# Kernel tuning notes

Measured on AMD Instinct MI355X. Metric: run time of the kernel, lower is better.

## Reference

```python
import jax, jax.numpy as jnp
import numpy as np

D, H = 1024, 8
HD = D // H           # head_dim = 128
M1 = 64               # att_mid_dim[1]
ALPHA = 1.3           # CELU alpha
EPS = 1e-5            # GroupNorm eps


def celu(x):
    return jnp.where(x > 0, x, ALPHA * jnp.expm1(x / ALPHA))


def group_norm(x, gamma, beta):
    # torch.nn.GroupNorm(H, D) on 2D input [N, D]: normalize within each group of HD channels
    N, C = x.shape
    xg = x.reshape(N, H, C // H)
    mu = xg.mean(-1, keepdims=True)
    var = xg.var(-1, keepdims=True)
    xn = ((xg - mu) * jax.lax.rsqrt(var + EPS)).reshape(N, C)
    return xn * gamma + beta


def branch(x, W, b, gamma, beta):
    # Linear -> CELU -> GroupNorm
    return group_norm(celu(x @ W + b), gamma, beta)


def setup_inputs() -> dict:
    key = jax.random.key(0)
    ks = jax.random.split(key, 24)
    B, M = 64, 1024
    s = 0.02
    inp = {
        "query": jax.random.normal(ks[0], (B, D), jnp.float32),
        "key": jax.random.normal(ks[1], (B, M, D), jnp.float32),
        "mask": jnp.ones((B, M), jnp.float32),
        "value1": jax.random.normal(ks[2], (B, D), jnp.float32),
        "value2": jax.random.normal(ks[3], (B, M, D), jnp.float32),
    }
    # four Linear+GroupNorm branches
    for i, name in enumerate(["q", "k", "v1", "v2"]):
        inp[f"W{name}"] = jax.random.normal(ks[4 + i], (D, D), jnp.float32) * s
        inp[f"b{name}"] = jnp.zeros((D,), jnp.float32)
        inp[f"g{name}"] = jnp.ones((D,), jnp.float32)
        inp[f"gb{name}"] = jnp.zeros((D,), jnp.float32)
    # SCAttention params: basic Linear(HD->M1), last Linear(M1->1), last2 Linear(M1->HD)
    inp["Wb"] = jax.random.normal(ks[10], (HD, M1), jnp.float32) * s
    inp["bb"] = jnp.zeros((M1,), jnp.float32)
    inp["Wl"] = jax.random.normal(ks[11], (M1, 1), jnp.float32) * s
    inp["bl"] = jnp.zeros((1,), jnp.float32)
    inp["Wl2"] = jax.random.normal(ks[12], (M1, HD), jnp.float32) * s
    inp["bl2"] = jnp.zeros((HD,), jnp.float32)
    return inp


def reference(query, key, mask, value1, value2,
              Wq, bq, gq, gbq, Wk, bk, gk, gbk,
              Wv1, bv1, gv1, gbv1, Wv2, bv2, gv2, gbv2,
              Wb, bb, Wl, bl, Wl2, bl2):
    B = query.shape[0]
    q = branch(query, Wq, bq, gq, gbq).reshape(B, H, HD)           # [B,H,HD]
    v1 = branch(value1, Wv1, bv1, gv1, gbv1).reshape(B, H, HD)     # [B,H,HD]
    k = branch(key.reshape(-1, D), Wk, bk, gk, gbk)
    k = k.reshape(B, -1, H, HD).transpose(0, 2, 1, 3)              # [B,H,M,HD]
    v2 = branch(value2.reshape(-1, D), Wv2, bv2, gv2, gbv2)
    v2 = v2.reshape(B, -1, H, HD).transpose(0, 2, 1, 3)            # [B,H,M,HD]

    attn_map = q[:, :, None, :] * k                                # Hadamard, [B,H,M,HD]

    # SCAttention (eval mode, dropout off)
    am = jax.nn.relu(attn_map @ Wb + bb)                           # [B,H,M,M1]
    mask_e = mask[:, None, :, None]                                # [B,1,M,1]
    am_pool = (am * mask_e).sum(-2) / mask_e.sum(-2)               # [B,H,M1]
    alpha_spatial = (am @ Wl + bl)[..., 0]                         # [B,H,M]
    alpha_channel = jax.nn.sigmoid(am_pool @ Wl2 + bl2)            # [B,H,HD]
    alpha_spatial = jnp.where(mask[:, None, :] == 0, -1e9, alpha_spatial)
    alpha_spatial = jax.nn.softmax(alpha_spatial, axis=-1)
    pooled_v2 = jnp.einsum('bhm,bhmd->bhd', alpha_spatial, v2)     # [B,H,HD]
    attn = v1 * pooled_v2 * alpha_channel                          # [B,H,HD]
    return attn.reshape(B, H * HD)
```

## Files before the change

### kernel.cpp

```cpp
#include <hip/hip_runtime.h>

typedef unsigned short u16;
typedef __attribute__((ext_vector_type(8))) short s16x8;
typedef __attribute__((ext_vector_type(8))) unsigned short u16x8;
typedef __attribute__((ext_vector_type(4))) float f32x4;

#define AS1 __attribute__((address_space(1)))
#define AS3 __attribute__((address_space(3)))

__device__ __forceinline__ float bf2f(u16 u) {
  union { unsigned u; float f; } x; x.u = ((unsigned)u) << 16; return x.f;
}
__device__ __forceinline__ u16 f2bf(float f) {
  union { float f; unsigned u; } x; x.f = f;
  unsigned r = x.u + 0x7fffu + ((x.u >> 16) & 1u);
  return (u16)(r >> 16);
}
__device__ __forceinline__ float celu_f(float x) {
  return x > 0.f ? x : 1.3f * expm1f(x * (1.0f / 1.3f));
}

__global__ __launch_bounds__(256) void convert_bf16(
    const float* __restrict__ X, u16* __restrict__ Y, long n)
{
  long i = ((long)blockIdx.x * 256 + threadIdx.x) * 8;
  const long stride = (long)gridDim.x * 256 * 8;
  for (; i < n; i += stride) {
    f32x4 a = *(const f32x4*)(X + i);
    f32x4 b = *(const f32x4*)(X + i + 4);
    u16x8 t;
#pragma unroll
    for (int e = 0; e < 4; ++e) { t[e] = f2bf(a[e]); t[4 + e] = f2bf(b[e]); }
    *(u16x8*)(Y + i) = t;
  }
}

__global__ __launch_bounds__(256) void transpose2_bf16(
    const float* __restrict__ W0, u16* __restrict__ WT0,
    const float* __restrict__ W1, u16* __restrict__ WT1)
{
  __shared__ float tile[32][33];
  const int bx = blockIdx.x;
  const int sel = blockIdx.y >> 5;
  const int by = blockIdx.y & 31;
  const float* W = sel ? W1 : W0;
  u16* WT = sel ? WT1 : WT0;
  const int tx = threadIdx.x, ty = threadIdx.y;
#pragma unroll
  for (int i = ty; i < 32; i += 8)
    tile[i][tx] = W[(by * 32 + i) * 1024 + bx * 32 + tx];
  __syncthreads();
#pragma unroll
  for (int i = ty; i < 32; i += 8)
    WT[(bx * 32 + i) * 1024 + by * 32 + tx] = f2bf(tile[tx][i]);
}

__global__ __launch_bounds__(256) void transpose_bf16(
    const float* __restrict__ W, u16* __restrict__ WT, int R, int C)
{
  __shared__ float tile[32][33];
  const int bx = blockIdx.x, by = blockIdx.y;
  const int tx = threadIdx.x, ty = threadIdx.y;
#pragma unroll
  for (int i = ty; i < 32; i += 8)
    tile[i][tx] = W[(by * 32 + i) * C + bx * 32 + tx];
  __syncthreads();
#pragma unroll
  for (int i = ty; i < 32; i += 8)
    WT[(bx * 32 + i) * R + by * 32 + tx] = f2bf(tile[tx][i]);
}

__global__ __launch_bounds__(128) void branch_small2(
    const float* __restrict__ X0, const float* __restrict__ W0,
    const float* __restrict__ b0, const float* __restrict__ g0,
    const float* __restrict__ be0, float* __restrict__ o0,
    const float* __restrict__ X1, const float* __restrict__ W1,
    const float* __restrict__ b1, const float* __restrict__ g1,
    const float* __restrict__ be1, float* __restrict__ o1)
{
  const int bid = blockIdx.x;
  const int sel = bid >> 9;
  const float* X = sel ? X1 : X0;  const float* W = sel ? W1 : W0;
  const float* bias = sel ? b1 : b0; const float* gamma = sel ? g1 : g0;
  const float* beta = sel ? be1 : be0; float* out = sel ? o1 : o0;
  const int b = (bid & 511) >> 3, grp = bid & 7;
  const int t = threadIdx.x;
  __shared__ float xs[1024];
  __shared__ float r1[2], r2[2];
  for (int i = t; i < 1024; i += 128) xs[i] = X[b * 1024 + i];
  __syncthreads();
  const int col = grp * 128 + t;
  const float* wp = W + col;
  float a0 = 0.f, a1 = 0.f, a2 = 0.f, a3 = 0.f;
  for (int k = 0; k < 1024; k += 4) {
    a0 += xs[k]     * wp[(k)     * 1024];
    a1 += xs[k + 1] * wp[(k + 1) * 1024];
    a2 += xs[k + 2] * wp[(k + 2) * 1024];
    a3 += xs[k + 3] * wp[(k + 3) * 1024];
  }
  float x = (a0 + a1) + (a2 + a3) + bias[col];
  float c = celu_f(x);
  float s1 = c, s2 = c * c;
#pragma unroll
  for (int m = 1; m < 64; m <<= 1) { s1 += __shfl_xor(s1, m); s2 += __shfl_xor(s2, m); }
  const int w = t >> 6;
  if ((t & 63) == 0) { r1[w] = s1; r2[w] = s2; }
  __syncthreads();
  float t1 = r1[0] + r1[1], t2 = r2[0] + r2[1];
  float mean = t1 * 0.0078125f;
  float var  = t2 * 0.0078125f - mean * mean;
  float inv  = rsqrtf(var + 1e-5f);
  out[b * 1024 + col] = (c - mean) * inv * gamma[col] + beta[col];
}

__global__ void
__attribute__((amdgpu_flat_work_group_size(512, 512), amdgpu_waves_per_eu(2, 2)))
gemm256p(
    const u16* __restrict__ A16, const u16* __restrict__ WT,
    const float* __restrict__ bias, const float* __restrict__ gamma,
    const float* __restrict__ beta, u16* __restrict__ Cout)
{
  __shared__ __align__(16) char lds_raw[143360];

  const int tid  = threadIdx.x;
  const int lane = tid & 63;
  const int w    = tid >> 6;
  const int wr   = w >> 2, wc = w & 3;
  const int lg   = lane >> 4, ln = lane & 15;

  const int bid = blockIdx.x;
  const int v   = (bid & 7) * 128 + (bid >> 3);
  const int mt  = v >> 2, nt = v & 3;

  const int trow = tid >> 3;
  const int gsw  = ((tid & 7) ^ (trow & 7)) * 8;
  const u16* aS00 = A16 + (long)(mt * 256 +   0 +  0 + trow) * 1024 + gsw;
  const u16* aS01 = A16 + (long)(mt * 256 +   0 + 64 + trow) * 1024 + gsw;
  const u16* aS10 = A16 + (long)(mt * 256 + 128 +  0 + trow) * 1024 + gsw;
  const u16* aS11 = A16 + (long)(mt * 256 + 128 + 64 + trow) * 1024 + gsw;
  const u16* bS0  = WT  + (long)(nt * 256 +   0 + trow) * 1024 + gsw;
  const u16* bS1  = WT  + (long)(nt * 256 +  64 + trow) * 1024 + gsw;
  const u16* bS2  = WT  + (long)(nt * 256 + 128 + trow) * 1024 + gsw;
  const u16* bS3  = WT  + (long)(nt * 256 + 192 + trow) * 1024 + gsw;

#define AQOFF(wr2, h, sl) ((((wr2) * 2 + (h)) * 2 + (sl)) * 8192)
#define BOFF(sl)          (65536 + (sl) * 32768)

#define AUP_STAGE(sl, kt)                                                       \
  { __builtin_amdgcn_global_load_lds((const AS1 void*)(aS01 + (kt) * 64),       \
        (AS3 void*)(lds_raw + AQOFF(0, 1, sl) + w * 1024), 16, 0, 0);           \
    __builtin_amdgcn_global_load_lds((const AS1 void*)(aS11 + (kt) * 64),       \
        (AS3 void*)(lds_raw + AQOFF(1, 1, sl) + w * 1024), 16, 0, 0); }
#define ALOW_STAGE(sl, kt)                                                      \
  { __builtin_amdgcn_global_load_lds((const AS1 void*)(aS00 + (kt) * 64),       \
        (AS3 void*)(lds_raw + AQOFF(0, 0, sl) + w * 1024), 16, 0, 0);           \
    __builtin_amdgcn_global_load_lds((const AS1 void*)(aS10 + (kt) * 64),       \
        (AS3 void*)(lds_raw + AQOFF(1, 0, sl) + w * 1024), 16, 0, 0); }
#define B_STAGE(sl, kt)                                                         \
  { __builtin_amdgcn_global_load_lds((const AS1 void*)(bS0 + (kt) * 64),        \
        (AS3 void*)(lds_raw + BOFF(sl) +     0 + w * 1024), 16, 0, 0);          \
    __builtin_amdgcn_global_load_lds((const AS1 void*)(bS1 + (kt) * 64),        \
        (AS3 void*)(lds_raw + BOFF(sl) +  8192 + w * 1024), 16, 0, 0);          \
    __builtin_amdgcn_global_load_lds((const AS1 void*)(bS2 + (kt) * 64),        \
        (AS3 void*)(lds_raw + BOFF(sl) + 16384 + w * 1024), 16, 0, 0);          \
    __builtin_amdgcn_global_load_lds((const AS1 void*)(bS3 + (kt) * 64),        \
        (AS3 void*)(lds_raw + BOFF(sl) + 24576 + w * 1024), 16, 0, 0); }

  int aoff0[4], aoff1[4], boff0[4], boff1[4];
#pragma unroll
  for (int la = 0; la < 4; ++la) {
    int rq = la * 16 + ln;
    aoff0[la] = rq * 128 + (((0 * 4 + lg) ^ (ln & 7)) * 16);
    aoff1[la] = rq * 128 + (((1 * 4 + lg) ^ (ln & 7)) * 16);
  }
#pragma unroll
  for (int j = 0; j < 4; ++j) {
    int nl = wc * 64 + j * 16 + ln;
    boff0[j] = nl * 128 + (((0 * 4 + lg) ^ (ln & 7)) * 16);
    boff1[j] = nl * 128 + (((1 * 4 + lg) ^ (ln & 7)) * 16);
  }

  f32x4 acc[8][4] = {};

#define MFMA_SET(IB, BF)                                                        \
    _Pragma("unroll")                                                           \
    for (int la = 0; la < 4; ++la)                                              \
      _Pragma("unroll")                                                         \
      for (int j = 0; j < 4; ++j)                                               \
        acc[(IB) + la][j] = __builtin_amdgcn_mfma_f32_16x16x32_bf16(            \
            afv[la], BF[j], acc[(IB) + la][j], 0, 0, 0);

#define KITER(T, STG, W1)                                                       \
  {                                                                             \
    const int slot = (T) & 1, nslot = slot ^ 1;                                 \
    const char* aqb0 = lds_raw + AQOFF(wr, 0, slot);                            \
    const char* aqb1 = lds_raw + AQOFF(wr, 1, slot);                            \
    const char* bqb  = lds_raw + BOFF(slot);                                    \
    s16x8 bfr[4], afv[4];                                                       \
    _Pragma("unroll")                                                           \
    for (int la = 0; la < 4; ++la) afv[la] = *(const s16x8*)(aqb0 + aoff0[la]); \
    _Pragma("unroll")                                                           \
    for (int j = 0; j < 4; ++j) bfr[j] = *(const s16x8*)(bqb + boff0[j]);       \
    if (STG) B_STAGE(nslot, (T) + 1);                                           \
    __builtin_amdgcn_s_barrier();                                               \
    asm volatile("s_waitcnt lgkmcnt(0)" ::);                                    \
    __builtin_amdgcn_sched_barrier(0);                                          \
    __builtin_amdgcn_s_setprio(1);                                              \
    MFMA_SET(0, bfr)                                                            \
    __builtin_amdgcn_s_setprio(0);                                              \
    asm volatile("s_waitcnt vmcnt(" #W1 ")" ::);                                \
    __builtin_amdgcn_sched_barrier(0);                                          \
    __builtin_amdgcn_s_barrier();                                               \
    __builtin_amdgcn_sched_barrier(0);                                          \
    _Pragma("unroll")                                                           \
    for (int la = 0; la < 4; ++la) afv[la] = *(const s16x8*)(aqb1 + aoff0[la]); \
    if (STG) ALOW_STAGE(nslot, (T) + 1);                                        \
    __builtin_amdgcn_s_barrier();                                               \
    asm volatile("s_waitcnt lgkmcnt(0)" ::);                                    \
    __builtin_amdgcn_sched_barrier(0);                                          \
    __builtin_amdgcn_s_setprio(1);                                              \
    MFMA_SET(4, bfr)                                                            \
    __builtin_amdgcn_s_setprio(0);                                              \
    __builtin_amdgcn_s_barrier();                                               \
    __builtin_amdgcn_sched_barrier(0);                                          \
    _Pragma("unroll")                                                           \
    for (int la = 0; la < 4; ++la) afv[la] = *(const s16x8*)(aqb0 + aoff1[la]); \
    _Pragma("unroll")                                                           \
    for (int j = 0; j < 4; ++j) bfr[j] = *(const s16x8*)(bqb + boff1[j]);       \
    if (STG) AUP_STAGE(nslot, (T) + 1);                                         \
    __builtin_amdgcn_s_barrier();                                               \
    asm volatile("s_waitcnt lgkmcnt(0)" ::);                                    \
    __builtin_amdgcn_sched_barrier(0);                                          \
    __builtin_amdgcn_s_setprio(1);                                              \
    MFMA_SET(0, bfr)                                                            \
    __builtin_amdgcn_s_setprio(0);                                              \
    __builtin_amdgcn_s_barrier();                                               \
    __builtin_amdgcn_sched_barrier(0);                                          \
    _Pragma("unroll")                                                           \
    for (int la = 0; la < 4; ++la) afv[la] = *(const s16x8*)(aqb1 + aoff1[la]); \
    __builtin_amdgcn_s_barrier();                                               \
    asm volatile("s_waitcnt lgkmcnt(0)" ::);                                    \
    __builtin_amdgcn_sched_barrier(0);                                          \
    __builtin_amdgcn_s_setprio(1);                                              \
    MFMA_SET(4, bfr)                                                            \
    __builtin_amdgcn_s_setprio(0);                                              \
    if (STG) { asm volatile("s_waitcnt vmcnt(2)" ::);                           \
               __builtin_amdgcn_sched_barrier(0); }                             \
    __builtin_amdgcn_s_barrier();                                               \
    __builtin_amdgcn_sched_barrier(0);                                          \
  }

  B_STAGE(0, 0);
  ALOW_STAGE(0, 0);
  AUP_STAGE(0, 0);
  asm volatile("s_waitcnt vmcnt(2)" ::);
  __builtin_amdgcn_sched_barrier(0);
  __builtin_amdgcn_s_barrier();
  __builtin_amdgcn_sched_barrier(0);

  for (int t = 0; t < 15; ++t)
    KITER(t, 1, 4)
  KITER(15, 0, 0)

#undef KITER
#undef MFMA_SET
#undef AUP_STAGE
#undef ALOW_STAGE
#undef B_STAGE
#undef AQOFF
#undef BOFF

  u16*   Csh = (u16*)lds_raw;
  float* red = (float*)(lds_raw + 135168);

  float bsv[4];
#pragma unroll
  for (int j = 0; j < 4; ++j) bsv[j] = bias[nt * 256 + wc * 64 + j * 16 + ln];

#pragma unroll
  for (int i = 0; i < 8; ++i) {
    float s1[4] = {0.f, 0.f, 0.f, 0.f}, s2[4] = {0.f, 0.f, 0.f, 0.f};
#pragma unroll
    for (int j = 0; j < 4; ++j) {
#pragma unroll
      for (int r = 0; r < 4; ++r) {
        float c = celu_f(acc[i][j][r] + bsv[j]);
        s1[r] += c; s2[r] += c * c;
        int rl = wr * 128 + i * 16 + 4 * lg + r;
        Csh[rl * 264 + wc * 64 + j * 16 + ln] = f2bf(c);
      }
    }
#pragma unroll
    for (int r = 0; r < 4; ++r) {
#pragma unroll
      for (int m = 1; m < 16; m <<= 1) {
        s1[r] += __shfl_xor(s1[r], m); s2[r] += __shfl_xor(s2[r], m);
      }
      if (ln == 0) {
        int rl = wr * 128 + i * 16 + 4 * lg + r;
        red[(rl * 4 + wc) * 2 + 0] = s1[r];
        red[(rl * 4 + wc) * 2 + 1] = s2[r];
      }
    }
  }
  __syncthreads();

  const int rsub = tid >> 5;
  const int cseg = (tid & 31) * 8;
  const int g2   = (cseg >> 7) * 2;
#pragma unroll 4
  for (int s = 0; s < 16; ++s) {
    int row_l = s * 16 + rsub;
    float s1t = red[(row_l * 4 + g2) * 2 + 0] + red[(row_l * 4 + g2 + 1) * 2 + 0];
    float s2t = red[(row_l * 4 + g2) * 2 + 1] + red[(row_l * 4 + g2 + 1) * 2 + 1];
    float mean = s1t * 0.0078125f;
    float var  = s2t * 0.0078125f - mean * mean;
    float inv  = rsqrtf(var + 1e-5f);
    u16x8 cv = *(const u16x8*)(Csh + row_l * 264 + cseg);
    int col0 = nt * 256 + cseg;
    f32x4 g0 = *(const f32x4*)(gamma + col0);
    f32x4 g1 = *(const f32x4*)(gamma + col0 + 4);
    f32x4 b0 = *(const f32x4*)(beta + col0);
    f32x4 b1 = *(const f32x4*)(beta + col0 + 4);
    u16x8 ov;
#pragma unroll
    for (int e = 0; e < 4; ++e) {
      ov[e]     = f2bf((bf2f(cv[e])     - mean) * inv * g0[e] + b0[e]);
      ov[4 + e] = f2bf((bf2f(cv[4 + e]) - mean) * inv * g1[e] + b1[e]);
    }
    *(u16x8*)(Cout + (long)(mt * 256 + row_l) * 1024 + col0) = ov;
  }
}

__global__ __launch_bounds__(256) void stage2(
    const float* __restrict__ qb, const float* __restrict__ v1b,
    const u16* __restrict__ kbuf, const u16* __restrict__ v2buf,
    const u16* __restrict__ wbT, const float* __restrict__ bb,
    const float* __restrict__ Wl, const float* __restrict__ bl,
    const float* __restrict__ Wl2, const float* __restrict__ bl2,
    const float* __restrict__ mask, float* __restrict__ out)
{
  const int bh = blockIdx.x, b = bh >> 3, h = bh & 7;
  const int tid = threadIdx.x, lane = tid & 63, w = tid >> 6;
  const int lg = lane >> 4, ln = lane & 15;

  __shared__ float s_arr[1024];
  __shared__ float pool_l[4][64];
  __shared__ float poolf[64];
  __shared__ float ach[128];
  __shared__ float psum2[4][128];
  __shared__ float rmsk[4], rmax[4], rsum[4];

  float qv[4][8];
#pragma unroll
  for (int ks = 0; ks < 4; ++ks)
#pragma unroll
    for (int e = 0; e < 8; ++e)
      qv[ks][e] = qb[b * 1024 + h * 128 + ks * 32 + lg * 8 + e];

  s16x8 bfr[4][4];
#pragma unroll
  for (int nj = 0; nj < 4; ++nj)
#pragma unroll
    for (int ks = 0; ks < 4; ++ks)
      bfr[nj][ks] = *(const s16x8*)(&wbT[(nj * 16 + ln) * 128 + ks * 32 + lg * 8]);

  float wlv[4], bbv[4];
#pragma unroll
  for (int nj = 0; nj < 4; ++nj) { wlv[nj] = Wl[nj * 16 + ln]; bbv[nj] = bb[nj * 16 + ln]; }

  float mpart = 0.f;
  for (int m = tid; m < 1024; m += 256) mpart += mask[b * 1024 + m];

  float poolacc[4] = {0.f, 0.f, 0.f, 0.f};

  for (int c = 0; c < 16; ++c) {
    const int m0 = w * 256 + c * 16;
    f32x4 amacc[4] = {};
#pragma unroll
    for (int ks = 0; ks < 4; ++ks) {
      const u16* kp = kbuf + (long)(b * 1024 + m0 + ln) * 1024 + h * 128 + ks * 32 + lg * 8;
      u16x8 kw = *(const u16x8*)kp;
      s16x8 af;
#pragma unroll
      for (int e = 0; e < 8; ++e) af[e] = (short)f2bf(bf2f(kw[e]) * qv[ks][e]);
#pragma unroll
      for (int nj = 0; nj < 4; ++nj)
        amacc[nj] = __builtin_amdgcn_mfma_f32_16x16x32_bf16(af, bfr[nj][ks], amacc[nj], 0, 0, 0);
    }
    float mrow[4];
#pragma unroll
    for (int r = 0; r < 4; ++r) mrow[r] = mask[b * 1024 + m0 + lg * 4 + r];
    float sp[4] = {0.f, 0.f, 0.f, 0.f};
#pragma unroll
    for (int nj = 0; nj < 4; ++nj)
#pragma unroll
      for (int r = 0; r < 4; ++r) {
        float a = fmaxf(amacc[nj][r] + bbv[nj], 0.f);
        poolacc[nj] += a * mrow[r];
        sp[r] += a * wlv[nj];
      }
#pragma unroll
    for (int m = 1; m < 16; m <<= 1)
#pragma unroll
      for (int r = 0; r < 4; ++r) sp[r] += __shfl_xor(sp[r], m);
    if (ln == 0) {
#pragma unroll
      for (int r = 0; r < 4; ++r) s_arr[m0 + lg * 4 + r] = sp[r] + bl[0];
    }
  }
#pragma unroll
  for (int m = 16; m < 64; m <<= 1)
#pragma unroll
    for (int nj = 0; nj < 4; ++nj) poolacc[nj] += __shfl_xor(poolacc[nj], m);
  if (lg == 0) {
#pragma unroll
    for (int nj = 0; nj < 4; ++nj) pool_l[w][nj * 16 + ln] = poolacc[nj];
  }
#pragma unroll
  for (int m = 1; m < 64; m <<= 1) mpart += __shfl_xor(mpart, m);
  if (lane == 0) rmsk[w] = mpart;
  __syncthreads();
  const float msum = rmsk[0] + rmsk[1] + rmsk[2] + rmsk[3];
  if (tid < 64) poolf[tid] = pool_l[0][tid] + pool_l[1][tid] + pool_l[2][tid] + pool_l[3][tid];
  float lmax = -3.0e38f;
  for (int m = tid; m < 1024; m += 256) {
    float sv = (mask[b * 1024 + m] == 0.f) ? -1.0e9f : s_arr[m];
    s_arr[m] = sv;
    lmax = fmaxf(lmax, sv);
  }
#pragma unroll
  for (int m = 1; m < 64; m <<= 1) lmax = fmaxf(lmax, __shfl_xor(lmax, m));
  if (lane == 0) rmax[w] = lmax;
  __syncthreads();
  const float gmax = fmaxf(fmaxf(rmax[0], rmax[1]), fmaxf(rmax[2], rmax[3]));
  float lsum = 0.f;
  for (int m = tid; m < 1024; m += 256) {
    float e = expf(s_arr[m] - gmax);
    s_arr[m] = e;
    lsum += e;
  }
#pragma unroll
  for (int m = 1; m < 64; m <<= 1) lsum += __shfl_xor(lsum, m);
  if (lane == 0) rsum[w] = lsum;
  if (tid < 128) {
    float a = 0.f;
    for (int cc = 0; cc < 64; ++cc) a += poolf[cc] * Wl2[cc * 128 + tid];
    a = a / msum + bl2[tid];
    ach[tid] = 1.f / (1.f + expf(-a));
  }
  __syncthreads();
  const float gsum = rsum[0] + rsum[1] + rsum[2] + rsum[3];

  float pacc[8] = {0.f, 0.f, 0.f, 0.f, 0.f, 0.f, 0.f, 0.f};
  const u16* vbase = v2buf + (long)(b * 1024 + w * 256) * 1024 + h * 128 + ln * 8;
#pragma unroll 4
  for (int i = 0; i < 64; ++i) {
    const int mrow = i * 4 + lg;
    u16x8 vv = *(const u16x8*)(vbase + (long)mrow * 1024);
    float s = s_arr[w * 256 + mrow];
#pragma unroll
    for (int e = 0; e < 8; ++e) pacc[e] += s * bf2f(vv[e]);
  }
#pragma unroll
  for (int e = 0; e < 8; ++e) {
    pacc[e] += __shfl_xor(pacc[e], 16);
    pacc[e] += __shfl_xor(pacc[e], 32);
  }
  if (lg == 0) {
    f32x4 p0 = {pacc[0], pacc[1], pacc[2], pacc[3]};
    f32x4 p1 = {pacc[4], pacc[5], pacc[6], pacc[7]};
    *(f32x4*)&psum2[w][ln * 8]     = p0;
    *(f32x4*)&psum2[w][ln * 8 + 4] = p1;
  }
  __syncthreads();
  if (tid < 128) {
    float pooled = (psum2[0][tid] + psum2[1][tid] + psum2[2][tid] + psum2[3][tid]) / gsum;
    out[b * 1024 + h * 128 + tid] = v1b[b * 1024 + h * 128 + tid] * pooled * ach[tid];
  }
}

extern "C" void kernel_launch(void* const* d_in, const int* in_sizes, int n_in,
                              void* d_out, int out_size, void* d_ws, size_t ws_size,
                              hipStream_t stream)
{
  (void)in_sizes; (void)n_in; (void)out_size; (void)ws_size;
  const float* query  = (const float*)d_in[0];
  const float* key    = (const float*)d_in[1];
  const float* mask   = (const float*)d_in[2];
  const float* value1 = (const float*)d_in[3];
  const float* value2 = (const float*)d_in[4];
  const float* Wq  = (const float*)d_in[5];
  const float* bq  = (const float*)d_in[6];
  const float* gq  = (const float*)d_in[7];
  const float* gbq = (const float*)d_in[8];
  const float* Wk  = (const float*)d_in[9];
  const float* bk  = (const float*)d_in[10];
  const float* gk  = (const float*)d_in[11];
  const float* gbk = (const float*)d_in[12];
  const float* Wv1  = (const float*)d_in[13];
  const float* bv1  = (const float*)d_in[14];
  const float* gv1  = (const float*)d_in[15];
  const float* gbv1 = (const float*)d_in[16];
  const float* Wv2  = (const float*)d_in[17];
  const float* bv2  = (const float*)d_in[18];
  const float* gv2  = (const float*)d_in[19];
  const float* gbv2 = (const float*)d_in[20];
  const float* Wb  = (const float*)d_in[21];
  const float* bb  = (const float*)d_in[22];
  const float* Wl  = (const float*)d_in[23];
  const float* bl  = (const float*)d_in[24];
  const float* Wl2 = (const float*)d_in[25];
  const float* bl2 = (const float*)d_in[26];
  float* out = (float*)d_out;

  char* ws = (char*)d_ws;
  const long SZ128 = 134217728L;
  u16*   convA  = (u16*)(ws);
  u16*   k_out  = (u16*)(ws + SZ128);
  u16*   v2_out = (u16*)(ws + 2 * SZ128);
  char*  wbase  = ws + 3 * SZ128;
  u16*   WkT    = (u16*)(wbase);
  u16*   Wv2T   = (u16*)(wbase + 2097152L);
  u16*   WbT    = (u16*)(wbase + 2L * 2097152L);
  float* qbuf   = (float*)(wbase + 2L * 2097152L + 32768L);
  float* v1buf  = (float*)(wbase + 2L * 2097152L + 32768L + 262144L);

  dim3 tb(32, 8);
  transpose2_bf16<<<dim3(32, 64), tb, 0, stream>>>(Wk, WkT, Wv2, Wv2T);
  transpose_bf16<<<dim3(2, 4), tb, 0, stream>>>(Wb, WbT, 128, 64);

  branch_small2<<<1024, 128, 0, stream>>>(query, Wq, bq, gq, gbq, qbuf,
                                          value1, Wv1, bv1, gv1, gbv1, v1buf);

  convert_bf16<<<4096, 256, 0, stream>>>(key, convA, 67108864L);
  gemm256p<<<1024, 512, 0, stream>>>(convA, WkT, bk, gk, gbk, k_out);

  convert_bf16<<<4096, 256, 0, stream>>>(value2, convA, 67108864L);
  gemm256p<<<1024, 512, 0, stream>>>(convA, Wv2T, bv2, gv2, gbv2, v2_out);

  stage2<<<512, 256, 0, stream>>>(qbuf, v1buf, k_out, v2_out, WbT,
                                  bb, Wl, bl, Wl2, bl2, mask, out);
}
```

Measured before the change: 683.5 us.

## Fuse fp32-to-bf16 conversion of activations into the GEMM A-tile staging

Removes the separate convert_bf16 passes over key and value2. The GEMM now loads fp32 A tiles into registers, converts them to bf16, and writes them into swizzled LDS, replacing the async global_load_lds path for A. This avoids writing and re-reading a 128MB bf16 intermediate per branch. In exchange, A loads become register-staged with extra VGPR pressure and conversion ALU work, and one of the per-iteration barriers becomes a full __syncthreads wait.

```diff
diff --git a/kernel.cpp b/kernel.cpp
--- a/kernel.cpp
+++ b/kernel.cpp
@@ -18,21 +18,6 @@
 }
 __device__ __forceinline__ float celu_f(float x) {
   return x > 0.f ? x : 1.3f * expm1f(x * (1.0f / 1.3f));
-}
-
-__global__ __launch_bounds__(256) void convert_bf16(
-    const float* __restrict__ X, u16* __restrict__ Y, long n)
-{
-  long i = ((long)blockIdx.x * 256 + threadIdx.x) * 8;
-  const long stride = (long)gridDim.x * 256 * 8;
-  for (; i < n; i += stride) {
-    f32x4 a = *(const f32x4*)(X + i);
-    f32x4 b = *(const f32x4*)(X + i + 4);
-    u16x8 t;
-#pragma unroll
-    for (int e = 0; e < 4; ++e) { t[e] = f2bf(a[e]); t[4 + e] = f2bf(b[e]); }
-    *(u16x8*)(Y + i) = t;
-  }
 }
 
 __global__ __launch_bounds__(256) void transpose2_bf16(
@@ -115,8 +100,8 @@
 
 __global__ void
 __attribute__((amdgpu_flat_work_group_size(512, 512), amdgpu_waves_per_eu(2, 2)))
-gemm256p(
-    const u16* __restrict__ A16, const u16* __restrict__ WT,
+gemm256f(
+    const float* __restrict__ A32, const u16* __restrict__ WT,
     const float* __restrict__ bias, const float* __restrict__ gamma,
     const float* __restrict__ beta, u16* __restrict__ Cout)
 {
@@ -132,30 +117,16 @@
   const int v   = (bid & 7) * 128 + (bid >> 3);
   const int mt  = v >> 2, nt = v & 3;
 
+#define AQOFF(wr2, h, sl) ((((wr2) * 2 + (h)) * 2 + (sl)) * 8192)
+#define BOFF(sl)          (65536 + (sl) * 32768)
+
   const int trow = tid >> 3;
   const int gsw  = ((tid & 7) ^ (trow & 7)) * 8;
-  const u16* aS00 = A16 + (long)(mt * 256 +   0 +  0 + trow) * 1024 + gsw;
-  const u16* aS01 = A16 + (long)(mt * 256 +   0 + 64 + trow) * 1024 + gsw;
-  const u16* aS10 = A16 + (long)(mt * 256 + 128 +  0 + trow) * 1024 + gsw;
-  const u16* aS11 = A16 + (long)(mt * 256 + 128 + 64 + trow) * 1024 + gsw;
-  const u16* bS0  = WT  + (long)(nt * 256 +   0 + trow) * 1024 + gsw;
-  const u16* bS1  = WT  + (long)(nt * 256 +  64 + trow) * 1024 + gsw;
-  const u16* bS2  = WT  + (long)(nt * 256 + 128 + trow) * 1024 + gsw;
-  const u16* bS3  = WT  + (long)(nt * 256 + 192 + trow) * 1024 + gsw;
-
-#define AQOFF(wr2, h, sl) ((((wr2) * 2 + (h)) * 2 + (sl)) * 8192)
-#define BOFF(sl)          (65536 + (sl) * 32768)
-
-#define AUP_STAGE(sl, kt)                                                       \
-  { __builtin_amdgcn_global_load_lds((const AS1 void*)(aS01 + (kt) * 64),       \
-        (AS3 void*)(lds_raw + AQOFF(0, 1, sl) + w * 1024), 16, 0, 0);           \
-    __builtin_amdgcn_global_load_lds((const AS1 void*)(aS11 + (kt) * 64),       \
-        (AS3 void*)(lds_raw + AQOFF(1, 1, sl) + w * 1024), 16, 0, 0); }
-#define ALOW_STAGE(sl, kt)                                                      \
-  { __builtin_amdgcn_global_load_lds((const AS1 void*)(aS00 + (kt) * 64),       \
-        (AS3 void*)(lds_raw + AQOFF(0, 0, sl) + w * 1024), 16, 0, 0);           \
-    __builtin_amdgcn_global_load_lds((const AS1 void*)(aS10 + (kt) * 64),       \
-        (AS3 void*)(lds_raw + AQOFF(1, 0, sl) + w * 1024), 16, 0, 0); }
+  const u16* bS0  = WT + (long)(nt * 256 +   0 + trow) * 1024 + gsw;
+  const u16* bS1  = WT + (long)(nt * 256 +  64 + trow) * 1024 + gsw;
+  const u16* bS2  = WT + (long)(nt * 256 + 128 + trow) * 1024 + gsw;
+  const u16* bS3  = WT + (long)(nt * 256 + 192 + trow) * 1024 + gsw;
+
 #define B_STAGE(sl, kt)                                                         \
   { __builtin_amdgcn_global_load_lds((const AS1 void*)(bS0 + (kt) * 64),        \
         (AS3 void*)(lds_raw + BOFF(sl) +     0 + w * 1024), 16, 0, 0);          \
@@ -166,6 +137,29 @@
     __builtin_amdgcn_global_load_lds((const AS1 void*)(bS3 + (kt) * 64),        \
         (AS3 void*)(lds_raw + BOFF(sl) + 24576 + w * 1024), 16, 0, 0); }
 
+  const int arow = tid >> 3;
+  const int acc_ = tid & 7;
+  const float* aR[4];
+  int awb[4];
+#pragma unroll
+  for (int s = 0; s < 4; ++s) {
+    int row_l = s * 64 + arow;
+    aR[s] = A32 + (long)(mt * 256 + row_l) * 1024 + acc_ * 8;
+    int q  = row_l >> 6;
+    int rq = row_l & 63;
+    awb[s] = q * 16384 + rq * 128 + ((acc_ ^ (rq & 7)) * 16);
+  }
+
+#define A_LOAD(AV, s, kt)                                                       \
+  { AV[2*(s)]   = *(const f32x4*)(aR[s] + (kt) * 64);                           \
+    AV[2*(s)+1] = *(const f32x4*)(aR[s] + (kt) * 64 + 4); }
+#define A_WRITE(AV, s, sl)                                                      \
+  { u16x8 tt;                                                                   \
+    _Pragma("unroll")                                                           \
+    for (int e = 0; e < 4; ++e) { tt[e] = f2bf(AV[2*(s)][e]);                   \
+                                  tt[4+e] = f2bf(AV[2*(s)+1][e]); }             \
+    *(u16x8*)(lds_raw + awb[s] + (sl) * 8192) = tt; }
+
   int aoff0[4], aoff1[4], boff0[4], boff1[4];
 #pragma unroll
   for (int la = 0; la < 4; ++la) {
@@ -190,31 +184,33 @@
         acc[(IB) + la][j] = __builtin_amdgcn_mfma_f32_16x16x32_bf16(            \
             afv[la], BF[j], acc[(IB) + la][j], 0, 0, 0);
 
-#define KITER(T, STG, W1)                                                       \
+#define KITER(T, STG)                                                           \
   {                                                                             \
     const int slot = (T) & 1, nslot = slot ^ 1;                                 \
     const char* aqb0 = lds_raw + AQOFF(wr, 0, slot);                            \
     const char* aqb1 = lds_raw + AQOFF(wr, 1, slot);                            \
     const char* bqb  = lds_raw + BOFF(slot);                                    \
     s16x8 bfr[4], afv[4];                                                       \
+    f32x4 av[8];                                                                \
+                      \
     _Pragma("unroll")                                                           \
     for (int la = 0; la < 4; ++la) afv[la] = *(const s16x8*)(aqb0 + aoff0[la]); \
     _Pragma("unroll")                                                           \
     for (int j = 0; j < 4; ++j) bfr[j] = *(const s16x8*)(bqb + boff0[j]);       \
-    if (STG) B_STAGE(nslot, (T) + 1);                                           \
+    if (STG) { B_STAGE(nslot, (T) + 1);                                         \
+               A_LOAD(av, 0, (T) + 1) A_LOAD(av, 1, (T) + 1) }                  \
     __builtin_amdgcn_s_barrier();                                               \
     asm volatile("s_waitcnt lgkmcnt(0)" ::);                                    \
     __builtin_amdgcn_sched_barrier(0);                                          \
     __builtin_amdgcn_s_setprio(1);                                              \
     MFMA_SET(0, bfr)                                                            \
     __builtin_amdgcn_s_setprio(0);                                              \
-    asm volatile("s_waitcnt vmcnt(" #W1 ")" ::);                                \
-    __builtin_amdgcn_sched_barrier(0);                                          \
-    __builtin_amdgcn_s_barrier();                                               \
-    __builtin_amdgcn_sched_barrier(0);                                          \
+    __builtin_amdgcn_s_barrier();                                               \
+    __builtin_amdgcn_sched_barrier(0);                                          \
+                                      \
     _Pragma("unroll")                                                           \
     for (int la = 0; la < 4; ++la) afv[la] = *(const s16x8*)(aqb1 + aoff0[la]); \
-    if (STG) ALOW_STAGE(nslot, (T) + 1);                                        \
+    if (STG) { A_LOAD(av, 2, (T) + 1) A_LOAD(av, 3, (T) + 1) }                  \
     __builtin_amdgcn_s_barrier();                                               \
     asm volatile("s_waitcnt lgkmcnt(0)" ::);                                    \
     __builtin_amdgcn_sched_barrier(0);                                          \
@@ -223,11 +219,12 @@
     __builtin_amdgcn_s_setprio(0);                                              \
     __builtin_amdgcn_s_barrier();                                               \
     __builtin_amdgcn_sched_barrier(0);                                          \
+                        \
     _Pragma("unroll")                                                           \
     for (int la = 0; la < 4; ++la) afv[la] = *(const s16x8*)(aqb0 + aoff1[la]); \
     _Pragma("unroll")                                                           \
     for (int j = 0; j < 4; ++j) bfr[j] = *(const s16x8*)(bqb + boff1[j]);       \
-    if (STG) AUP_STAGE(nslot, (T) + 1);                                         \
+    if (STG) { A_WRITE(av, 0, nslot) A_WRITE(av, 1, nslot) }                    \
     __builtin_amdgcn_s_barrier();                                               \
     asm volatile("s_waitcnt lgkmcnt(0)" ::);                                    \
     __builtin_amdgcn_sched_barrier(0);                                          \
@@ -236,36 +233,36 @@
     __builtin_amdgcn_s_setprio(0);                                              \
     __builtin_amdgcn_s_barrier();                                               \
     __builtin_amdgcn_sched_barrier(0);                                          \
+                         \
     _Pragma("unroll")                                                           \
     for (int la = 0; la < 4; ++la) afv[la] = *(const s16x8*)(aqb1 + aoff1[la]); \
+    if (STG) { A_WRITE(av, 2, nslot) A_WRITE(av, 3, nslot) }                    \
     __builtin_amdgcn_s_barrier();                                               \
     asm volatile("s_waitcnt lgkmcnt(0)" ::);                                    \
     __builtin_amdgcn_sched_barrier(0);                                          \
     __builtin_amdgcn_s_setprio(1);                                              \
     MFMA_SET(4, bfr)                                                            \
     __builtin_amdgcn_s_setprio(0);                                              \
-    if (STG) { asm volatile("s_waitcnt vmcnt(2)" ::);                           \
-               __builtin_amdgcn_sched_barrier(0); }                             \
-    __builtin_amdgcn_s_barrier();                                               \
-    __builtin_amdgcn_sched_barrier(0);                                          \
-  }
-
-  B_STAGE(0, 0);
-  ALOW_STAGE(0, 0);
-  AUP_STAGE(0, 0);
-  asm volatile("s_waitcnt vmcnt(2)" ::);
-  __builtin_amdgcn_sched_barrier(0);
-  __builtin_amdgcn_s_barrier();
-  __builtin_amdgcn_sched_barrier(0);
+    __syncthreads();   \
+    __builtin_amdgcn_sched_barrier(0);                                          \
+  }
+
+  {
+    B_STAGE(0, 0);
+    f32x4 av[8];
+    A_LOAD(av, 0, 0) A_LOAD(av, 1, 0) A_LOAD(av, 2, 0) A_LOAD(av, 3, 0)
+    A_WRITE(av, 0, 0) A_WRITE(av, 1, 0) A_WRITE(av, 2, 0) A_WRITE(av, 3, 0)
+    __syncthreads();
+  }
 
   for (int t = 0; t < 15; ++t)
-    KITER(t, 1, 4)
-  KITER(15, 0, 0)
+    KITER(t, 1)
+  KITER(15, 0)
 
 #undef KITER
 #undef MFMA_SET
-#undef AUP_STAGE
-#undef ALOW_STAGE
+#undef A_LOAD
+#undef A_WRITE
 #undef B_STAGE
 #undef AQOFF
 #undef BOFF
@@ -516,10 +513,9 @@
 
   char* ws = (char*)d_ws;
   const long SZ128 = 134217728L;
-  u16*   convA  = (u16*)(ws);
-  u16*   k_out  = (u16*)(ws + SZ128);
-  u16*   v2_out = (u16*)(ws + 2 * SZ128);
-  char*  wbase  = ws + 3 * SZ128;
+  u16*   k_out  = (u16*)(ws);
+  u16*   v2_out = (u16*)(ws + SZ128);
+  char*  wbase  = ws + 2 * SZ128;
   u16*   WkT    = (u16*)(wbase);
   u16*   Wv2T   = (u16*)(wbase + 2097152L);
   u16*   WbT    = (u16*)(wbase + 2L * 2097152L);
@@ -533,11 +529,8 @@
   branch_small2<<<1024, 128, 0, stream>>>(query, Wq, bq, gq, gbq, qbuf,
                                           value1, Wv1, bv1, gv1, gbv1, v1buf);
 
-  convert_bf16<<<4096, 256, 0, stream>>>(key, convA, 67108864L);
-  gemm256p<<<1024, 512, 0, stream>>>(convA, WkT, bk, gk, gbk, k_out);
-
-  convert_bf16<<<4096, 256, 0, stream>>>(value2, convA, 67108864L);
-  gemm256p<<<1024, 512, 0, stream>>>(convA, Wv2T, bv2, gv2, gbv2, v2_out);
+  gemm256f<<<1024, 512, 0, stream>>>(key,    WkT,  bk,  gk,  gbk,  k_out);
+  gemm256f<<<1024, 512, 0, stream>>>(value2, Wv2T, bv2, gv2, gbv2, v2_out);
 
   stage2<<<512, 256, 0, stream>>>(qbuf, v1buf, k_out, v2_out, WbT,
                                   bb, Wl, bl, Wl2, bl2, mask, out);
```

New measurement: 730.8 us. 6.9% more time.

## Simplify GEMM pipeline to one bulk prefetch and one barrier per k-step

Applied to the files above, without the earlier changes.

The bf16 GEMM main loop is rebuilt so that every global-to-LDS load for the next k-tile (A and B) is issued at the start of each iteration. All four MFMA sub-blocks then run without intermediate s_barriers, and a single __syncthreads closes each iteration. This replaces the staggered staging of B, A-low and A-high and the many barriers that kept the waves in lockstep. It is meant to cut barrier and synchronisation overhead. In exchange it loses the tuned wave ping-pong and finer-grained load/compute interleaving, and relies on __syncthreads to wait for the async LDS loads.

```diff
diff --git a/kernel.cpp b/kernel.cpp
--- a/kernel.cpp
+++ b/kernel.cpp
@@ -115,7 +115,7 @@
 
 __global__ void
 __attribute__((amdgpu_flat_work_group_size(512, 512), amdgpu_waves_per_eu(2, 2)))
-gemm256p(
+gemm256p2(
     const u16* __restrict__ A16, const u16* __restrict__ WT,
     const float* __restrict__ bias, const float* __restrict__ gamma,
     const float* __restrict__ beta, u16* __restrict__ Cout)
@@ -146,17 +146,7 @@
 #define AQOFF(wr2, h, sl) ((((wr2) * 2 + (h)) * 2 + (sl)) * 8192)
 #define BOFF(sl)          (65536 + (sl) * 32768)
 
-#define AUP_STAGE(sl, kt)                                                       \
-  { __builtin_amdgcn_global_load_lds((const AS1 void*)(aS01 + (kt) * 64),       \
-        (AS3 void*)(lds_raw + AQOFF(0, 1, sl) + w * 1024), 16, 0, 0);           \
-    __builtin_amdgcn_global_load_lds((const AS1 void*)(aS11 + (kt) * 64),       \
-        (AS3 void*)(lds_raw + AQOFF(1, 1, sl) + w * 1024), 16, 0, 0); }
-#define ALOW_STAGE(sl, kt)                                                      \
-  { __builtin_amdgcn_global_load_lds((const AS1 void*)(aS00 + (kt) * 64),       \
-        (AS3 void*)(lds_raw + AQOFF(0, 0, sl) + w * 1024), 16, 0, 0);           \
-    __builtin_amdgcn_global_load_lds((const AS1 void*)(aS10 + (kt) * 64),       \
-        (AS3 void*)(lds_raw + AQOFF(1, 0, sl) + w * 1024), 16, 0, 0); }
-#define B_STAGE(sl, kt)                                                         \
+#define STAGE_ALL(sl, kt)                                                       \
   { __builtin_amdgcn_global_load_lds((const AS1 void*)(bS0 + (kt) * 64),        \
         (AS3 void*)(lds_raw + BOFF(sl) +     0 + w * 1024), 16, 0, 0);          \
     __builtin_amdgcn_global_load_lds((const AS1 void*)(bS1 + (kt) * 64),        \
@@ -164,7 +154,15 @@
     __builtin_amdgcn_global_load_lds((const AS1 void*)(bS2 + (kt) * 64),        \
         (AS3 void*)(lds_raw + BOFF(sl) + 16384 + w * 1024), 16, 0, 0);          \
     __builtin_amdgcn_global_load_lds((const AS1 void*)(bS3 + (kt) * 64),        \
-        (AS3 void*)(lds_raw + BOFF(sl) + 24576 + w * 1024), 16, 0, 0); }
+        (AS3 void*)(lds_raw + BOFF(sl) + 24576 + w * 1024), 16, 0, 0);          \
+    __builtin_amdgcn_global_load_lds((const AS1 void*)(aS00 + (kt) * 64),       \
+        (AS3 void*)(lds_raw + AQOFF(0, 0, sl) + w * 1024), 16, 0, 0);           \
+    __builtin_amdgcn_global_load_lds((const AS1 void*)(aS10 + (kt) * 64),       \
+        (AS3 void*)(lds_raw + AQOFF(1, 0, sl) + w * 1024), 16, 0, 0);           \
+    __builtin_amdgcn_global_load_lds((const AS1 void*)(aS01 + (kt) * 64),       \
+        (AS3 void*)(lds_raw + AQOFF(0, 1, sl) + w * 1024), 16, 0, 0);           \
+    __builtin_amdgcn_global_load_lds((const AS1 void*)(aS11 + (kt) * 64),       \
+        (AS3 void*)(lds_raw + AQOFF(1, 1, sl) + w * 1024), 16, 0, 0); }
 
   int aoff0[4], aoff1[4], boff0[4], boff1[4];
 #pragma unroll
@@ -190,83 +188,63 @@
         acc[(IB) + la][j] = __builtin_amdgcn_mfma_f32_16x16x32_bf16(            \
             afv[la], BF[j], acc[(IB) + la][j], 0, 0, 0);
 
-#define KITER(T, STG, W1)                                                       \
+#define KITER(T, STG)                                                           \
   {                                                                             \
     const int slot = (T) & 1, nslot = slot ^ 1;                                 \
     const char* aqb0 = lds_raw + AQOFF(wr, 0, slot);                            \
     const char* aqb1 = lds_raw + AQOFF(wr, 1, slot);                            \
     const char* bqb  = lds_raw + BOFF(slot);                                    \
     s16x8 bfr[4], afv[4];                                                       \
+    if (STG) STAGE_ALL(nslot, (T) + 1);                                         \
+                                                      \
     _Pragma("unroll")                                                           \
     for (int la = 0; la < 4; ++la) afv[la] = *(const s16x8*)(aqb0 + aoff0[la]); \
     _Pragma("unroll")                                                           \
     for (int j = 0; j < 4; ++j) bfr[j] = *(const s16x8*)(bqb + boff0[j]);       \
-    if (STG) B_STAGE(nslot, (T) + 1);                                           \
-    __builtin_amdgcn_s_barrier();                                               \
     asm volatile("s_waitcnt lgkmcnt(0)" ::);                                    \
     __builtin_amdgcn_sched_barrier(0);                                          \
     __builtin_amdgcn_s_setprio(1);                                              \
     MFMA_SET(0, bfr)                                                            \
     __builtin_amdgcn_s_setprio(0);                                              \
-    asm volatile("s_waitcnt vmcnt(" #W1 ")" ::);                                \
-    __builtin_amdgcn_sched_barrier(0);                                          \
-    __builtin_amdgcn_s_barrier();                                               \
-    __builtin_amdgcn_sched_barrier(0);                                          \
+                                                       \
     _Pragma("unroll")                                                           \
     for (int la = 0; la < 4; ++la) afv[la] = *(const s16x8*)(aqb1 + aoff0[la]); \
-    if (STG) ALOW_STAGE(nslot, (T) + 1);                                        \
-    __builtin_amdgcn_s_barrier();                                               \
     asm volatile("s_waitcnt lgkmcnt(0)" ::);                                    \
     __builtin_amdgcn_sched_barrier(0);                                          \
     __builtin_amdgcn_s_setprio(1);                                              \
     MFMA_SET(4, bfr)                                                            \
     __builtin_amdgcn_s_setprio(0);                                              \
-    __builtin_amdgcn_s_barrier();                                               \
-    __builtin_amdgcn_sched_barrier(0);                                          \
+                                                      \
     _Pragma("unroll")                                                           \
     for (int la = 0; la < 4; ++la) afv[la] = *(const s16x8*)(aqb0 + aoff1[la]); \
     _Pragma("unroll")                                                           \
     for (int j = 0; j < 4; ++j) bfr[j] = *(const s16x8*)(bqb + boff1[j]);       \
-    if (STG) AUP_STAGE(nslot, (T) + 1);                                         \
-    __builtin_amdgcn_s_barrier();                                               \
     asm volatile("s_waitcnt lgkmcnt(0)" ::);                                    \
     __builtin_amdgcn_sched_barrier(0);                                          \
     __builtin_amdgcn_s_setprio(1);                                              \
     MFMA_SET(0, bfr)                                                            \
     __builtin_amdgcn_s_setprio(0);                                              \
-    __builtin_amdgcn_s_barrier();                                               \
-    __builtin_amdgcn_sched_barrier(0);                                          \
+                                                       \
     _Pragma("unroll")                                                           \
     for (int la = 0; la < 4; ++la) afv[la] = *(const s16x8*)(aqb1 + aoff1[la]); \
-    __builtin_amdgcn_s_barrier();                                               \
     asm volatile("s_waitcnt lgkmcnt(0)" ::);                                    \
     __builtin_amdgcn_sched_barrier(0);                                          \
     __builtin_amdgcn_s_setprio(1);                                              \
     MFMA_SET(4, bfr)                                                            \
     __builtin_amdgcn_s_setprio(0);                                              \
-    if (STG) { asm volatile("s_waitcnt vmcnt(2)" ::);                           \
-               __builtin_amdgcn_sched_barrier(0); }                             \
-    __builtin_amdgcn_s_barrier();                                               \
-    __builtin_amdgcn_sched_barrier(0);                                          \
-  }
-
-  B_STAGE(0, 0);
-  ALOW_STAGE(0, 0);
-  AUP_STAGE(0, 0);
-  asm volatile("s_waitcnt vmcnt(2)" ::);
-  __builtin_amdgcn_sched_barrier(0);
-  __builtin_amdgcn_s_barrier();
-  __builtin_amdgcn_sched_barrier(0);
+    __syncthreads();   \
+  }
+
+  STAGE_ALL(0, 0);
+  __syncthreads();
 
   for (int t = 0; t < 15; ++t)
-    KITER(t, 1, 4)
-  KITER(15, 0, 0)
+    KITER(t, 1)
+  KITER(15, 0)
 
 #undef KITER
 #undef MFMA_SET
-#undef AUP_STAGE
-#undef ALOW_STAGE
-#undef B_STAGE
+#undef STAGE_ALL
 #undef AQOFF
 #undef BOFF
 
@@ -534,10 +512,10 @@
                                           value1, Wv1, bv1, gv1, gbv1, v1buf);
 
   convert_bf16<<<4096, 256, 0, stream>>>(key, convA, 67108864L);
-  gemm256p<<<1024, 512, 0, stream>>>(convA, WkT, bk, gk, gbk, k_out);
+  gemm256p2<<<1024, 512, 0, stream>>>(convA, WkT, bk, gk, gbk, k_out);
 
   convert_bf16<<<4096, 256, 0, stream>>>(value2, convA, 67108864L);
-  gemm256p<<<1024, 512, 0, stream>>>(convA, Wv2T, bv2, gv2, gbv2, v2_out);
+  gemm256p2<<<1024, 512, 0, stream>>>(convA, Wv2T, bv2, gv2, gbv2, v2_out);
 
   stage2<<<512, 256, 0, stream>>>(qbuf, v1buf, k_out, v2_out, WbT,
                                   bb, Wl, bl, Wl2, bl2, mask, out);
```

Result: no change. 690.3 us (+1.0%).
